# Performance work log

Measured on AMD Instinct MI355X. Metric: run time of the kernel, lower is better.

The kernel has to match this reference:

```python
import jax, jax.numpy as jnp
import numpy as np

N_NODES = 50000
N_EDGES = 1600000
D_IN = 128
D_HID = 128


def setup_inputs() -> dict:
    key = jax.random.key(0)
    ks = jax.random.split(key, 6)
    edge_index = jax.random.randint(ks[0], (2, N_EDGES), 0, N_NODES, dtype=jnp.int32)
    emb = jax.random.normal(ks[1], (N_NODES, D_IN), dtype=jnp.float32) * 0.1
    W1 = jax.random.normal(ks[2], (D_IN, D_HID), dtype=jnp.float32) * (1.0 / np.sqrt(D_IN))
    b1 = jnp.zeros((D_HID,), dtype=jnp.float32)
    W2 = jax.random.normal(ks[3], (D_HID, D_HID), dtype=jnp.float32) * (1.0 / np.sqrt(D_HID))
    b2 = jnp.zeros((D_HID,), dtype=jnp.float32)
    head_w = jax.random.normal(ks[4], (D_HID, 1), dtype=jnp.float32) * (1.0 / np.sqrt(D_HID))
    head_b = jnp.zeros((1,), dtype=jnp.float32)
    return {"edge_index": edge_index, "emb": emb, "W1": W1, "b1": b1,
            "W2": W2, "b2": b2, "head_w": head_w, "head_b": head_b}


def _gcn_norm(edge_index, num_nodes):
    # PyG GCNConv default: add self-loops, sym-normalize D^-1/2 (A+I) D^-1/2.
    loops = jnp.arange(num_nodes, dtype=edge_index.dtype)
    src = jnp.concatenate([edge_index[0], loops])  # [E+N]
    dst = jnp.concatenate([edge_index[1], loops])  # [E+N]
    deg = jax.ops.segment_sum(jnp.ones_like(dst, dtype=jnp.float32), dst,
                              num_segments=num_nodes)  # [N], >=1 via self-loops
    dis = jax.lax.rsqrt(deg)
    norm = dis[src] * dis[dst]  # [E+N]
    return src, dst, norm


def _gcn_conv(x, W, b, src, dst, norm, num_nodes):
    h = x @ W                                  # [N, D] dense transform first
    msg = h[src] * norm[:, None]               # [E+N, D] gather + scale
    out = jax.ops.segment_sum(msg, dst, num_segments=num_nodes)  # scatter-add
    return out + b


def reference(edge_index, emb, W1, b1, W2, b2, head_w, head_b):
    src, dst, norm = _gcn_norm(edge_index, N_NODES)
    x = jax.nn.relu(_gcn_conv(emb, W1, b1, src, dst, norm, N_NODES))
    x = jax.nn.relu(_gcn_conv(x, W2, b2, src, dst, norm, N_NODES))
    scores = jax.nn.sigmoid(x @ head_w + head_b)[:, 0]  # [N]
    return scores
```

## Files before the change

### kernel.cpp

```cpp
#include <hip/hip_runtime.h>
#include <hip/hip_fp16.h>
#include <math.h>

#define D 128
#define D4 32
#define AP 136
#define AP8 144
#define NBUCK 512
#define NT 512
#define EPB 4096
#define BCAP2 4096

typedef _Float16 f16x8 __attribute__((ext_vector_type(8)));
typedef float f32x4 __attribute__((ext_vector_type(4)));
typedef float f32x2 __attribute__((ext_vector_type(2)));


__global__ void prep_all_kernel(const float* __restrict__ W1, _Float16* __restrict__ Wt1,
                                const float* __restrict__ W2, _Float16* __restrict__ Wt2,
                                int* __restrict__ bcnt) {
    int t = threadIdx.x;
    if (blockIdx.x == 0) { bcnt[t] = 0; bcnt[256 + t] = 0; }
    int half = blockIdx.x & 63;
    const float* W = (blockIdx.x < 64) ? W1 : W2;
    _Float16* Wt   = (blockIdx.x < 64) ? Wt1 : Wt2;
    int i = half * 256 + t;
    int k = i >> 7, c = i & 127;
    Wt[c * 128 + k] = (_Float16)W[i];
}


__global__ __launch_bounds__(NT) void bucket_pass1(const int* __restrict__ src,
                                                   const int* __restrict__ dst,
                                                   int* __restrict__ bcnt,
                                                   unsigned* __restrict__ buckets,
                                                   int E, unsigned magicM) {
    __shared__ unsigned stage[EPB];
    __shared__ int lcnt[NBUCK], loff[NBUCK], gbase[NBUCK];

    int t = threadIdx.x;
    int base = blockIdx.x * EPB;
    int nblk = min(EPB, E - base);
    lcnt[t] = 0;
    __syncthreads();

    for (int i = t; i < nblk; i += NT) {
        unsigned d = (unsigned)dst[base + i];
        int b = (int)(((unsigned long long)d * magicM) >> 24);
        atomicAdd(&lcnt[b], 1);
    }
    __syncthreads();

    int v = lcnt[t];
    loff[t] = v;
    __syncthreads();
    for (int off = 1; off < NT; off <<= 1) {
        int x = (t >= off) ? loff[t - off] : 0;
        __syncthreads();
        loff[t] += x;
        __syncthreads();
    }
    int incl = loff[t];
    __syncthreads();
    loff[t] = incl - v;
    gbase[t] = atomicAdd(&bcnt[t], v);
    lcnt[t] = 0;
    __syncthreads();

    for (int i = t; i < nblk; i += NT) {
        unsigned s = (unsigned)src[base + i];
        unsigned d = (unsigned)dst[base + i];
        unsigned pk = (s << 16) | d;
        int b = (int)(((unsigned long long)d * magicM) >> 24);
        int p = atomicAdd(&lcnt[b], 1);
        stage[loff[b] + p] = pk;
    }
    __syncthreads();

    for (int i = t; i < nblk; i += NT) {
        unsigned pk = stage[i];
        int b = (int)(((unsigned long long)(pk & 0xffffu) * magicM) >> 24);
        int pos = gbase[b] + (i - loff[b]);
        if (pos < BCAP2) buckets[(size_t)b * BCAP2 + pos] = pk;
    }
}

__global__ __launch_bounds__(NT) void csr_pass2(const unsigned* __restrict__ buckets,
                                                const int* __restrict__ bcnt,
                                                int* __restrict__ row_ptr,
                                                float* __restrict__ dis,
                                                unsigned short* __restrict__ col,
                                                int N, int npb, int E) {
    __shared__ int cnt[NT], sc[NT], excl[NT];
    __shared__ unsigned short estage[BCAP2];

    int b = blockIdx.x;
    int t = threadIdx.x;

    int bv = min(bcnt[t], BCAP2);
    sc[t] = bv;
    __syncthreads();
    for (int off = 1; off < NT; off <<= 1) {
        int x = (t >= off) ? sc[t - off] : 0;
        __syncthreads();
        sc[t] += x;
        __syncthreads();
    }
    int base = sc[b] - min(bcnt[b], BCAP2);
    if (b == 0 && t == 0) row_ptr[N] = E;
    __syncthreads();

    int lo = b * npb;
    int nn = min(npb, N - lo);
    int n = min(bcnt[b], BCAP2);
    const unsigned* bk = buckets + (size_t)b * BCAP2;

    cnt[t] = 0;
    __syncthreads();
    for (int i = t; i < n; i += NT) {
        int dl = (int)(bk[i] & 0xffffu) - lo;
        atomicAdd(&cnt[dl], 1);
    }
    __syncthreads();
    int v = cnt[t];
    sc[t] = v;
    __syncthreads();
    for (int off = 1; off < NT; off <<= 1) {
        int x = (t >= off) ? sc[t - off] : 0;
        __syncthreads();
        sc[t] += x;
        __syncthreads();
    }
    excl[t] = sc[t] - v;
    if (t < nn) {
        row_ptr[lo + t] = base + excl[t];
        dis[lo + t] = rsqrtf((float)v + 1.0f);
    }
    cnt[t] = 0;
    __syncthreads();
    for (int i = t; i < n; i += NT) {
        unsigned pk = bk[i];
        int dl = (int)(pk & 0xffffu) - lo;
        int p = atomicAdd(&cnt[dl], 1);
        estage[excl[dl] + p] = (unsigned short)(pk >> 16);
    }
    __syncthreads();
    for (int i = t; i < n; i += NT) col[base + i] = estage[i];
}


#define GEMM_CORE                                                            \
    const uint4* Wt16 = (const uint4*)Wt;                                    \
    for (int i = t; i < 128 * 16; i += 256) {                                \
        int r = i >> 4, ch = i & 15;                                         \
        *(uint4*)&Ws[r * AP + ch * 8] = Wt16[i];                             \
    }                                                                        \
    __syncthreads();                                                         \
    int wave = t >> 6;                                                       \
    int lane = t & 63;                                                       \
    int m16 = lane & 15;                                                     \
    int quad = lane >> 4;                                                    \
    f32x4 acc[8];                                                            \
    for (int n = 0; n < 8; n++) acc[n] = (f32x4){0.f, 0.f, 0.f, 0.f};        \
    _Pragma("unroll")                                                        \
    for (int kc = 0; kc < 4; kc++) {                                         \
        f16x8 a = *(const f16x8*)&As[(wave * 16 + m16) * AP + kc * 32 + quad * 8]; \
        _Pragma("unroll")                                                    \
        for (int n = 0; n < 8; n++) {                                        \
            f16x8 bfrag = *(const f16x8*)&Ws[(n * 16 + m16) * AP + kc * 32 + quad * 8]; \
            acc[n] = __builtin_amdgcn_mfma_f32_16x16x32_f16(a, bfrag, acc[n], 0, 0, 0); \
        }                                                                    \
    }                                                                        \
    __syncthreads();                                                         \
    unsigned char* Cs8 = (unsigned char*)As;                                 \
    float dv[4];                                                             \
    _Pragma("unroll")                                                        \
    for (int r = 0; r < 4; r++) {                                            \
        int grow = row0 + wave * 16 + quad * 4 + r;                          \
        dv[r] = (grow < N) ? dis[grow] : 0.f;                                \
    }                                                                        \
    _Pragma("unroll")                                                        \
    for (int n = 0; n < 8; n++)                                              \
        _Pragma("unroll")                                                    \
        for (int r = 0; r < 4; r++) {                                        \
            float val = acc[n][r] * dv[r];                                   \
            int wq = __builtin_amdgcn_cvt_pk_fp8_f32(val, val, 0, false);    \
            Cs8[(wave * 16 + quad * 4 + r) * AP8 + n * 16 + m16] = (unsigned char)(wq & 0xff); \
        }                                                                    \
    __syncthreads();                                                         \
    uint4* C16 = (uint4*)C8;                                                 \
    for (int i = lane; i < 128; i += 64) {                                   \
        int r = i >> 3, ch = i & 7;                                          \
        int grow = row0 + wave * 16 + r;                                     \
        if (grow < N)                                                        \
            C16[(size_t)grow * 8 + ch] = *(const uint4*)&Cs8[(wave * 16 + r) * AP8 + ch * 16]; \
    }

__global__ __launch_bounds__(256) void gemm_f32a_fp8c(const float* __restrict__ A,
                                                      const _Float16* __restrict__ Wt,
                                                      const float* __restrict__ dis,
                                                      unsigned int* __restrict__ C8, int N) {
    __shared__ _Float16 As[64 * AP];
    __shared__ _Float16 Ws[128 * AP];
    int t = threadIdx.x;
    int row0 = blockIdx.x * 64;
    const float4* A4 = (const float4*)A;
    for (int i = t; i < 64 * 16; i += 256) {
        int r = i >> 4, ch = i & 15;
        uint4 v = make_uint4(0, 0, 0, 0);
        if (row0 + r < N) {
            float4 a0 = A4[(size_t)(row0 + r) * 32 + ch * 2];
            float4 a1 = A4[(size_t)(row0 + r) * 32 + ch * 2 + 1];
            __half2 h0 = __floats2half2_rn(a0.x, a0.y);
            __half2 h1 = __floats2half2_rn(a0.z, a0.w);
            __half2 h2 = __floats2half2_rn(a1.x, a1.y);
            __half2 h3 = __floats2half2_rn(a1.z, a1.w);
            v.x = *(unsigned*)&h0; v.y = *(unsigned*)&h1;
            v.z = *(unsigned*)&h2; v.w = *(unsigned*)&h3;
        }
        *(uint4*)&As[r * AP + ch * 8] = v;
    }
    GEMM_CORE
}

__global__ __launch_bounds__(256) void gemm_f16a_fp8c(const _Float16* __restrict__ A,
                                                      const _Float16* __restrict__ Wt,
                                                      const float* __restrict__ dis,
                                                      unsigned int* __restrict__ C8, int N) {
    __shared__ _Float16 As[64 * AP];
    __shared__ _Float16 Ws[128 * AP];
    int t = threadIdx.x;
    int row0 = blockIdx.x * 64;
    const uint4* A16 = (const uint4*)A;
    for (int i = t; i < 64 * 16; i += 256) {
        int r = i >> 4, ch = i & 15;
        uint4 v = make_uint4(0, 0, 0, 0);
        if (row0 + r < N) v = A16[(size_t)(row0 + r) * 16 + ch];
        *(uint4*)&As[r * AP + ch * 8] = v;
    }
    GEMM_CORE
}


__device__ __forceinline__ void acc8(float4& a, unsigned int u) {
    f32x2 lo = __builtin_amdgcn_cvt_pk_f32_fp8((int)u, false);
    f32x2 hi = __builtin_amdgcn_cvt_pk_f32_fp8((int)u, true);
    a.x += lo[0]; a.y += lo[1]; a.z += hi[0]; a.w += hi[1];
}

#define AGG8_BODY                                                               \
    float4 acc = make_float4(0.f, 0.f, 0.f, 0.f);                               \
    acc8(acc, t8[(size_t)node * D4 + lane]);        \
    int e0 = row_ptr[node], e1 = row_ptr[node + 1];                             \
    int deg = e1 - e0;                                                          \
    for (int base = 0; base < deg; base += 32) {                                \
        int cnt = min(32, deg - base);                                          \
        int myc = (base + lane < deg) ? (int)col[e0 + base + lane] : 0;         \
        int j = 0;                                                              \
        for (; j + 8 <= cnt; j += 8) {                                          \
            int s0 = __shfl(myc, j + 0, 32); int s1 = __shfl(myc, j + 1, 32);   \
            int s2 = __shfl(myc, j + 2, 32); int s3 = __shfl(myc, j + 3, 32);   \
            int s4 = __shfl(myc, j + 4, 32); int s5 = __shfl(myc, j + 5, 32);   \
            int s6 = __shfl(myc, j + 6, 32); int s7 = __shfl(myc, j + 7, 32);   \
            unsigned int u0 = t8[(size_t)s0 * D4 + lane];                       \
            unsigned int u1 = t8[(size_t)s1 * D4 + lane];                       \
            unsigned int u2 = t8[(size_t)s2 * D4 + lane];                       \
            unsigned int u3 = t8[(size_t)s3 * D4 + lane];                       \
            unsigned int u4 = t8[(size_t)s4 * D4 + lane];                       \
            unsigned int u5 = t8[(size_t)s5 * D4 + lane];                       \
            unsigned int u6 = t8[(size_t)s6 * D4 + lane];                       \
            unsigned int u7 = t8[(size_t)s7 * D4 + lane];                       \
            acc8(acc, u0); acc8(acc, u1); acc8(acc, u2); acc8(acc, u3);         \
            acc8(acc, u4); acc8(acc, u5); acc8(acc, u6); acc8(acc, u7);         \
        }                                                                       \
        for (; j < cnt; j++) {                                                  \
            int s = __shfl(myc, j, 32);                                         \
            acc8(acc, t8[(size_t)s * D4 + lane]);                               \
        }                                                                       \
    }                                                                           \
    float di = dis[node];                                                       \
    float4 bb = ((const float4*)bias)[lane];                                    \
    float4 o;                                                                   \
    o.x = fmaxf(fmaf(di, acc.x, bb.x), 0.f);                                    \
    o.y = fmaxf(fmaf(di, acc.y, bb.y), 0.f);                                    \
    o.z = fmaxf(fmaf(di, acc.z, bb.z), 0.f);                                    \
    o.w = fmaxf(fmaf(di, acc.w, bb.w), 0.f);

__global__ void agg_fp8_kernel(const unsigned int* __restrict__ t8, const float* __restrict__ bias,
                               const int* __restrict__ row_ptr, const unsigned short* __restrict__ col,
                               const float* __restrict__ dis, _Float16* __restrict__ xout, int N) {
    int t = threadIdx.x;
    int node = blockIdx.x * 8 + (t >> 5);
    int lane = t & 31;
    if (node >= N) return;
    AGG8_BODY
    __half2 q0 = __floats2half2_rn(o.x, o.y);
    __half2 q1 = __floats2half2_rn(o.z, o.w);
    uint2 u;
    u.x = *(unsigned int*)&q0;
    u.y = *(unsigned int*)&q1;
    ((uint2*)xout)[(size_t)node * D4 + lane] = u;
}

__global__ void agg_head_fp8_kernel(const unsigned int* __restrict__ t8, const float* __restrict__ bias,
                                    const int* __restrict__ row_ptr, const unsigned short* __restrict__ col,
                                    const float* __restrict__ dis,
                                    const float* __restrict__ head_w, const float* __restrict__ head_b,
                                    float* __restrict__ out, int N) {
    int t = threadIdx.x;
    int node = blockIdx.x * 8 + (t >> 5);
    int lane = t & 31;
    if (node >= N) return;
    AGG8_BODY
    float4 wv = ((const float4*)head_w)[lane];
    float s = o.x * wv.x + o.y * wv.y + o.z * wv.z + o.w * wv.w;
    for (int m = 1; m < 32; m <<= 1) s += __shfl_xor(s, m, 64);
    if (lane == 0) {
        float v = s + head_b[0];
        out[node] = 1.0f / (1.0f + expf(-v));
    }
}


extern "C" void kernel_launch(void* const* d_in, const int* in_sizes, int n_in,
                              void* d_out, int out_size, void* d_ws, size_t ws_size,
                              hipStream_t stream) {
    const int*   edge   = (const int*)d_in[0];
    const float* emb    = (const float*)d_in[1];
    const float* W1     = (const float*)d_in[2];
    const float* b1     = (const float*)d_in[3];
    const float* W2     = (const float*)d_in[4];
    const float* b2     = (const float*)d_in[5];
    const float* head_w = (const float*)d_in[6];
    const float* head_b = (const float*)d_in[7];
    float* out = (float*)d_out;

    int E = in_sizes[0] / 2;
    int N = in_sizes[1] / D;
    const int* srcp = edge;
    const int* dstp = edge + E;

    char* w = (char*)d_ws;
    auto alloc = [&](size_t bytes) -> char* {
        char* p = w;
        w += (bytes + 15) & ~(size_t)15;
        return p;
    };
    unsigned int*   t8      = (unsigned int*)alloc((size_t)N * D);
    _Float16*       x1h     = (_Float16*)alloc((size_t)N * D * 2);
    unsigned*       buckets = (unsigned*)alloc((size_t)NBUCK * BCAP2 * 4);
    _Float16*       Wt1     = (_Float16*)alloc((size_t)D * D * 2);
    _Float16*       Wt2     = (_Float16*)alloc((size_t)D * D * 2);
    unsigned short* col     = (unsigned short*)alloc((size_t)E * 2);
    int*            bcnt    = (int*)alloc(NBUCK * 4);
    int*            row_ptr = (int*)alloc((size_t)(N + 1) * 4);
    float*          dis     = (float*)alloc((size_t)N * 4);

    int npb = (N + NBUCK - 1) / NBUCK;
    unsigned magicM = (16777216u + (unsigned)npb - 1) / (unsigned)npb;
    int gP1 = (E + EPB - 1) / EPB;
    int gG = (N + 63) / 64;
    int gA = (N + 7) / 8;

    prep_all_kernel<<<128, 256, 0, stream>>>(W1, Wt1, W2, Wt2, bcnt);
    bucket_pass1<<<gP1, NT, 0, stream>>>(srcp, dstp, bcnt, buckets, E, magicM);
    csr_pass2<<<NBUCK, NT, 0, stream>>>(buckets, bcnt, row_ptr, dis, col, N, npb, E);

    gemm_f32a_fp8c<<<gG, 256, 0, stream>>>(emb, Wt1, dis, t8, N);
    agg_fp8_kernel<<<gA, 256, 0, stream>>>(t8, b1, row_ptr, col, dis, x1h, N);
    gemm_f16a_fp8c<<<gG, 256, 0, stream>>>(x1h, Wt2, dis, t8, N);
    agg_head_fp8_kernel<<<gA, 256, 0, stream>>>(t8, b2, row_ptr, col, dis,
                                                head_w, head_b, out, N);
}
```

Before: 194.9 us.

## Split each CSR row by source half to improve gather locality

The CSR build now splits each node's neighbor list into sources below N/2 and sources at or above N/2, and records a per-row midpoint. Aggregation walks the two ranges separately, so concurrent waves gather from one half of the feature table at a time, which is meant to improve cache hit rates. This adds extra shared-memory atomics in csr_pass2, a row_mid array, and a second partial 32-wide chunk per node. EPB is also halved, doubling the number of pass-1 blocks.

```diff
diff --git a/kernel.cpp b/kernel.cpp
--- a/kernel.cpp
+++ b/kernel.cpp
@@ -8,7 +8,7 @@
 #define AP8 144
 #define NBUCK 512
 #define NT 512
-#define EPB 4096
+#define EPB 2048
 #define BCAP2 4096
 
 typedef _Float16 f16x8 __attribute__((ext_vector_type(8)));
@@ -88,10 +88,11 @@
 __global__ __launch_bounds__(NT) void csr_pass2(const unsigned* __restrict__ buckets,
                                                 const int* __restrict__ bcnt,
                                                 int* __restrict__ row_ptr,
+                                                int* __restrict__ row_mid,
                                                 float* __restrict__ dis,
                                                 unsigned short* __restrict__ col,
-                                                int N, int npb, int E) {
-    __shared__ int cnt[NT], sc[NT], excl[NT];
+                                                int N, int npb, int E, int mid) {
+    __shared__ int cnt[NT], cntA[NT], sc[NT], excl[NT], curA[NT], curB[NT];
     __shared__ unsigned short estage[BCAP2];
 
     int b = blockIdx.x;
@@ -116,10 +117,13 @@
     const unsigned* bk = buckets + (size_t)b * BCAP2;
 
     cnt[t] = 0;
+    cntA[t] = 0;
     __syncthreads();
     for (int i = t; i < n; i += NT) {
-        int dl = (int)(bk[i] & 0xffffu) - lo;
+        unsigned pk = bk[i];
+        int dl = (int)(pk & 0xffffu) - lo;
         atomicAdd(&cnt[dl], 1);
+        if ((int)(pk >> 16) < mid) atomicAdd(&cntA[dl], 1);
     }
     __syncthreads();
     int v = cnt[t];
@@ -134,15 +138,20 @@
     excl[t] = sc[t] - v;
     if (t < nn) {
         row_ptr[lo + t] = base + excl[t];
+        row_mid[lo + t] = base + excl[t] + cntA[t];
         dis[lo + t] = rsqrtf((float)v + 1.0f);
     }
-    cnt[t] = 0;
+    curA[t] = 0;
+    curB[t] = 0;
     __syncthreads();
     for (int i = t; i < n; i += NT) {
         unsigned pk = bk[i];
         int dl = (int)(pk & 0xffffu) - lo;
-        int p = atomicAdd(&cnt[dl], 1);
-        estage[excl[dl] + p] = (unsigned short)(pk >> 16);
+        int s = (int)(pk >> 16);
+        int p;
+        if (s < mid) p = excl[dl] + atomicAdd(&curA[dl], 1);
+        else         p = excl[dl] + cntA[dl] + atomicAdd(&curB[dl], 1);
+        estage[p] = (unsigned short)s;
     }
     __syncthreads();
     for (int i = t; i < n; i += NT) col[base + i] = estage[i];
@@ -248,14 +257,10 @@
     a.x += lo[0]; a.y += lo[1]; a.z += hi[0]; a.w += hi[1];
 }
 
-#define AGG8_BODY                                                               \
-    float4 acc = make_float4(0.f, 0.f, 0.f, 0.f);                               \
-    acc8(acc, t8[(size_t)node * D4 + lane]);        \
-    int e0 = row_ptr[node], e1 = row_ptr[node + 1];                             \
-    int deg = e1 - e0;                                                          \
-    for (int base = 0; base < deg; base += 32) {                                \
-        int cnt = min(32, deg - base);                                          \
-        int myc = (base + lane < deg) ? (int)col[e0 + base + lane] : 0;         \
+#define AGG_RANGE(lo_, hi_)                                                     \
+    for (int base = (lo_); base < (hi_); base += 32) {                          \
+        int cnt = min(32, (hi_) - base);                                        \
+        int myc = (base + lane < (hi_)) ? (int)col[base + lane] : 0;            \
         int j = 0;                                                              \
         for (; j + 8 <= cnt; j += 8) {                                          \
             int s0 = __shfl(myc, j + 0, 32); int s1 = __shfl(myc, j + 1, 32);   \
@@ -277,7 +282,15 @@
             int s = __shfl(myc, j, 32);                                         \
             acc8(acc, t8[(size_t)s * D4 + lane]);                               \
         }                                                                       \
-    }                                                                           \
+    }
+
+#define AGG8_BODY                                                               \
+    float4 acc = make_float4(0.f, 0.f, 0.f, 0.f);                               \
+    acc8(acc, t8[(size_t)node * D4 + lane]);        \
+    int e0 = row_ptr[node], e1 = row_ptr[node + 1];                             \
+    int em = row_mid[node];                                                     \
+    AGG_RANGE(e0, em)                \
+    AGG_RANGE(em, e1)               \
     float di = dis[node];                                                       \
     float4 bb = ((const float4*)bias)[lane];                                    \
     float4 o;                                                                   \
@@ -287,7 +300,8 @@
     o.w = fmaxf(fmaf(di, acc.w, bb.w), 0.f);
 
 __global__ void agg_fp8_kernel(const unsigned int* __restrict__ t8, const float* __restrict__ bias,
-                               const int* __restrict__ row_ptr, const unsigned short* __restrict__ col,
+                               const int* __restrict__ row_ptr, const int* __restrict__ row_mid,
+                               const unsigned short* __restrict__ col,
                                const float* __restrict__ dis, _Float16* __restrict__ xout, int N) {
     int t = threadIdx.x;
     int node = blockIdx.x * 8 + (t >> 5);
@@ -303,7 +317,8 @@
 }
 
 __global__ void agg_head_fp8_kernel(const unsigned int* __restrict__ t8, const float* __restrict__ bias,
-                                    const int* __restrict__ row_ptr, const unsigned short* __restrict__ col,
+                                    const int* __restrict__ row_ptr, const int* __restrict__ row_mid,
+                                    const unsigned short* __restrict__ col,
                                     const float* __restrict__ dis,
                                     const float* __restrict__ head_w, const float* __restrict__ head_b,
                                     float* __restrict__ out, int N) {
@@ -354,21 +369,23 @@
     unsigned short* col     = (unsigned short*)alloc((size_t)E * 2);
     int*            bcnt    = (int*)alloc(NBUCK * 4);
     int*            row_ptr = (int*)alloc((size_t)(N + 1) * 4);
+    int*            row_mid = (int*)alloc((size_t)N * 4);
     float*          dis     = (float*)alloc((size_t)N * 4);
 
     int npb = (N + NBUCK - 1) / NBUCK;
     unsigned magicM = (16777216u + (unsigned)npb - 1) / (unsigned)npb;
+    int mid = N / 2;
     int gP1 = (E + EPB - 1) / EPB;
     int gG = (N + 63) / 64;
     int gA = (N + 7) / 8;
 
     prep_all_kernel<<<128, 256, 0, stream>>>(W1, Wt1, W2, Wt2, bcnt);
     bucket_pass1<<<gP1, NT, 0, stream>>>(srcp, dstp, bcnt, buckets, E, magicM);
-    csr_pass2<<<NBUCK, NT, 0, stream>>>(buckets, bcnt, row_ptr, dis, col, N, npb, E);
+    csr_pass2<<<NBUCK, NT, 0, stream>>>(buckets, bcnt, row_ptr, row_mid, dis, col, N, npb, E, mid);
 
     gemm_f32a_fp8c<<<gG, 256, 0, stream>>>(emb, Wt1, dis, t8, N);
-    agg_fp8_kernel<<<gA, 256, 0, stream>>>(t8, b1, row_ptr, col, dis, x1h, N);
+    agg_fp8_kernel<<<gA, 256, 0, stream>>>(t8, b1, row_ptr, row_mid, col, dis, x1h, N);
     gemm_f16a_fp8c<<<gG, 256, 0, stream>>>(x1h, Wt2, dis, t8, N);
-    agg_head_fp8_kernel<<<gA, 256, 0, stream>>>(t8, b2, row_ptr, col, dis,
+    agg_head_fp8_kernel<<<gA, 256, 0, stream>>>(t8, b2, row_ptr, row_mid, col, dis,
                                                 head_w, head_b, out, N);
 }
```

New measurement: 209.2 us. 1.07x slower.
